# Kernel tuning notes

Hardware: AMD Instinct MI355X
Metric: run time of the kernel (lower is better)

## Reference

```python
import jax, jax.numpy as jnp
import numpy as np

NUM_HEADS = 2
ROPE_BASE = 10000.0


def _rope_tables(seq_len, head_dim, dtype):
    # inv_freq over even indices of head_dim
    inv_freq = 1.0 / (ROPE_BASE ** (jnp.arange(0, head_dim, 2, dtype=jnp.float32) / head_dim))
    t = jnp.arange(seq_len, dtype=jnp.float32)
    freqs = t[:, None] * inv_freq[None, :]            # (s, head_dim/2)
    emb = jnp.concatenate([freqs, freqs], axis=-1)    # (s, head_dim)
    return jnp.cos(emb).astype(dtype), jnp.sin(emb).astype(dtype)


def _apply_rotation(x_bsd, cos, sin):
    # x_bsd: (b, s, h*d); chunk in half along last dim (h=2 -> halves == head_dim)
    x1, x2 = jnp.split(x_bsd, 2, axis=-1)
    return jnp.concatenate([x1 * cos - x2 * sin, x2 * cos + x1 * sin], axis=-1)


def setup_inputs() -> dict:
    key = jax.random.key(0)
    k1, k2, k3, k4 = jax.random.split(key, 4)
    b, s, dim = 4, 2048, 2048
    x = jax.random.normal(k1, (b, s, dim), dtype=jnp.float32)
    wqkv = jax.random.normal(k2, (dim, 3 * dim), dtype=jnp.float32) * (dim ** -0.5)
    wout = jax.random.normal(k3, (dim, dim), dtype=jnp.float32) * (dim ** -0.5)
    bout = jax.random.normal(k4, (dim,), dtype=jnp.float32) * 0.01
    return {"x": x, "wqkv": wqkv, "wout": wout, "bout": bout}


def reference(x, wqkv, wout, bout):
    b, s, dim = x.shape
    h = NUM_HEADS
    d = dim // h
    scale = d ** -0.5

    qkv = x @ wqkv                                    # (b, s, 3*dim)
    qkv = qkv.reshape(b, s, 3, h, d).transpose(2, 0, 3, 1, 4)  # (3, b, h, s, d)
    q, k, v = qkv[0], qkv[1], qkv[2]                  # (b, h, s, d)

    # RoPE applied on (b, s, h*d) layout, exactly as source
    cos, sin = _rope_tables(s, d, x.dtype)            # (s, d) each
    q_flat = q.transpose(0, 2, 1, 3).reshape(b, s, h * d)
    k_flat = k.transpose(0, 2, 1, 3).reshape(b, s, h * d)
    q = _apply_rotation(q_flat, cos, sin).reshape(b, s, h, d).transpose(0, 2, 1, 3)
    k = _apply_rotation(k_flat, cos, sin).reshape(b, s, h, d).transpose(0, 2, 1, 3)

    scores = jnp.einsum('bhid,bhjd->bhij', q, k) * scale
    attn = jax.nn.softmax(scores, axis=-1)
    out = jnp.einsum('bhij,bhjd->bhid', attn, v)      # (b, h, s, d)
    out = out.transpose(0, 2, 1, 3).reshape(b, s, dim)
    return out @ wout + bout
```

## Files before the change

### kernel.cpp

```cpp
#include <hip/hip_runtime.h>
#include <hip/hip_fp16.h>

typedef __attribute__((ext_vector_type(4))) float f32x4;
typedef __attribute__((ext_vector_type(8))) _Float16 f16x8;
typedef __attribute__((ext_vector_type(4))) _Float16 f16x4;

__device__ __forceinline__ void gload_lds16(const void* gp, void* lp) {
    __builtin_amdgcn_global_load_lds(
        (const __attribute__((address_space(1))) void*)gp,
        (__attribute__((address_space(3))) void*)lp, 16, 0, 0);
}

__global__ void f32_to_f16_vec(const float* __restrict__ in, _Float16* __restrict__ out) {
    long i = ((long)blockIdx.x * 256 + threadIdx.x) * 4;
    f32x4 v = *(const f32x4*)(in + i);
    f16x4 h;
#pragma unroll
    for (int e = 0; e < 4; ++e) h[e] = (_Float16)v[e];
    *(f16x4*)(out + i) = h;
}

__global__ void transpose_f32_to_f16(const float* __restrict__ in, _Float16* __restrict__ out,
                                     int R, int C) {
    __shared__ _Float16 tile[32][36];
    const int c0 = blockIdx.x * 32, r0 = blockIdx.y * 32;
    const int t = threadIdx.x;
    const int r = t >> 3, c4 = (t & 7) * 4;
    f32x4 v = *(const f32x4*)(in + (long)(r0 + r) * C + c0 + c4);
    f16x4 h;
#pragma unroll
    for (int e = 0; e < 4; ++e) h[e] = (_Float16)v[e];
    *(f16x4*)&tile[r][c4] = h;
    __syncthreads();
    const int oc = t >> 3, o4 = (t & 7) * 4;
    f16x4 o;
#pragma unroll
    for (int e = 0; e < 4; ++e) o[e] = tile[o4 + e][oc];
    *(f16x4*)(out + (long)(c0 + oc) * R + r0 + o4) = o;
}

__global__ void rope_inplace(_Float16* __restrict__ qkv) {
    const int row = blockIdx.x;
    const int s = row & 2047;
    const int j0 = threadIdx.x * 4;
    _Float16* base = qkv + (long)row * 6144;
    f16x4 q0 = *(const f16x4*)(base + j0);
    f16x4 q1 = *(const f16x4*)(base + 1024 + j0);
    f16x4 k0 = *(const f16x4*)(base + 2048 + j0);
    f16x4 k1 = *(const f16x4*)(base + 3072 + j0);
    f16x4 oq0, oq1, ok0, ok1;
#pragma unroll
    for (int e = 0; e < 4; ++e) {
        int fi = (j0 + e) & 511;
        float expo = (float)(2 * fi) * (1.0f / 1024.0f);
        float invf = 1.0f / powf(10000.0f, expo);
        float ang = (float)s * invf;
        float sn, cs;
        sincosf(ang, &sn, &cs);
        float a = (float)q0[e], b = (float)q1[e];
        oq0[e] = (_Float16)(a * cs - b * sn);
        oq1[e] = (_Float16)(b * cs + a * sn);
        float c = (float)k0[e], d = (float)k1[e];
        ok0[e] = (_Float16)(c * cs - d * sn);
        ok1[e] = (_Float16)(d * cs + c * sn);
    }
    *(f16x4*)(base + j0) = oq0;
    *(f16x4*)(base + 1024 + j0) = oq1;
    *(f16x4*)(base + 2048 + j0) = ok0;
    *(f16x4*)(base + 3072 + j0) = ok1;
}

__global__ void v_transpose(const _Float16* __restrict__ qkv, _Float16* __restrict__ vT) {
    __shared__ _Float16 tile[32][36];
    const int z = blockIdx.z, b = z >> 1, h = z & 1;
    const int s0 = blockIdx.x * 32, d0 = blockIdx.y * 32;
    const int t = threadIdx.x;
    const int r = t >> 3, c4 = (t & 7) * 4;
    const _Float16* src = qkv + (long)(b * 2048 + s0 + r) * 6144 + 4096 + h * 1024 + d0 + c4;
    *(f16x4*)&tile[r][c4] = *(const f16x4*)src;
    __syncthreads();
    const int dr = t >> 3, sc = (t & 7) * 4;
    f16x4 o;
#pragma unroll
    for (int e = 0; e < 4; ++e) o[e] = tile[sc + e][dr];
    *(f16x4*)(vT + ((long)z * 1024 + d0 + dr) * 2048 + s0 + sc) = o;
}

__global__ __launch_bounds__(256) void softmax_rows_f32(float* __restrict__ S, float scale) {
    const int wid = threadIdx.x >> 6, lane = threadIdx.x & 63;
    const long row = (long)blockIdx.x * 4 + wid;
    float* rp = S + row * 2048;
    f32x4 v[8];
    float mx = -1e30f;
#pragma unroll
    for (int i = 0; i < 8; ++i) {
        v[i] = *(const f32x4*)(rp + (i * 64 + lane) * 4);
#pragma unroll
        for (int e = 0; e < 4; ++e) mx = fmaxf(mx, v[i][e]);
    }
#pragma unroll
    for (int o = 32; o > 0; o >>= 1) mx = fmaxf(mx, __shfl_xor(mx, o, 64));
    float sum = 0.f;
#pragma unroll
    for (int i = 0; i < 8; ++i)
#pragma unroll
        for (int e = 0; e < 4; ++e) {
            float p = __expf(scale * (v[i][e] - mx));
            v[i][e] = p; sum += p;
        }
#pragma unroll
    for (int o = 32; o > 0; o >>= 1) sum += __shfl_xor(sum, o, 64);
    float inv = 1.0f / sum;
    _Float16* wp = (_Float16*)S + row * 4096;
#pragma unroll
    for (int i = 0; i < 8; ++i) {
        f16x4 h;
#pragma unroll
        for (int e = 0; e < 4; ++e) h[e] = (_Float16)(v[i][e] * inv);
        *(f16x4*)(wp + (i * 64 + lane) * 4) = h;
    }
}

__global__ __launch_bounds__(256) void softmax_rows_f16(_Float16* __restrict__ S, float scale) {
    const int wid = threadIdx.x >> 6, lane = threadIdx.x & 63;
    const long row = (long)blockIdx.x * 4 + wid;
    _Float16* rp = S + row * 2048;
    f16x8 v[4];
    float f[32];
    float mx = -1e30f;
#pragma unroll
    for (int i = 0; i < 4; ++i) {
        v[i] = *(const f16x8*)(rp + i * 512 + lane * 8);
#pragma unroll
        for (int e = 0; e < 8; ++e) {
            f[i * 8 + e] = (float)v[i][e];
            mx = fmaxf(mx, f[i * 8 + e]);
        }
    }
#pragma unroll
    for (int o = 32; o > 0; o >>= 1) mx = fmaxf(mx, __shfl_xor(mx, o, 64));
    float sum = 0.f;
#pragma unroll
    for (int i = 0; i < 32; ++i) {
        float p = __expf(scale * (f[i] - mx));
        f[i] = p; sum += p;
    }
#pragma unroll
    for (int o = 32; o > 0; o >>= 1) sum += __shfl_xor(sum, o, 64);
    float inv = 1.0f / sum;
#pragma unroll
    for (int i = 0; i < 4; ++i) {
        f16x8 h;
#pragma unroll
        for (int e = 0; e < 8; ++e) h[e] = (_Float16)(f[i * 8 + e] * inv);
        *(f16x8*)(rp + i * 512 + lane * 8) = h;
    }
}

template <bool OUT_F16, bool BIAS>
__global__ __launch_bounds__(512, 2)
void gemm256(const _Float16* __restrict__ A, const _Float16* __restrict__ B,
             void* __restrict__ Cv, const float* __restrict__ bias,
             int K, int lda, int ldb, int ldc, int zmod,
             long a1, long a2, long b1, long b2, long c1, long c2) {
    __shared__ char lds[131072];
    const int z = blockIdx.z, zq = z / zmod, zr = z - zq * zmod;
    A += zq * a1 + zr * a2;
    B += zq * b1 + zr * b2;
    const long coff = zq * c1 + zr * c2;
    const int tm = blockIdx.y * 256, tn = blockIdx.x * 256;
    const int t = threadIdx.x;
    const int lane = t & 63, wid = t >> 6;
    const int wr = wid >> 2, wc = wid & 3;
    const int fr = lane & 15;

    const int scol = 8 * ((lane & 3) ^ ((lane >> 3) & 3));
    const int srow = wid * 32 + (lane >> 2);
    const _Float16* gA = A + (long)(tm + srow) * lda + scol;
    const _Float16* gB = B + (long)(tn + srow) * ldb + scol;
    char* lA = lds + wid * 2048;
    char* lB = lds + 65536 + wid * 2048;

    const int gsw = 16 * ((lane >> 4) ^ ((fr >> 1) & 3));
    const int aoff = (wr * 128 + fr) * 64 + gsw;
    const int boff = 65536 + (wc * 64 + fr) * 64 + gsw;

    const int NT = K >> 5;
    f32x4 acc[8][4] = {};

    auto stageA = [&](int tt) {
        const int so = (tt & 3) * 16384;
        const long ko = (long)tt * 32;
        gload_lds16(gA + ko, lA + so);
        gload_lds16(gA + ko + (long)16 * lda, lA + so + 1024);
    };
    auto stageB = [&](int tt) {
        const int so = (tt & 3) * 16384;
        const long ko = (long)tt * 32;
        gload_lds16(gB + ko, lB + so);
        gload_lds16(gB + ko + (long)16 * ldb, lB + so + 1024);
    };

    stageA(0); stageB(0); stageA(1); stageB(1); stageA(2); stageB(2);

    for (int tt = 0; tt < NT; ++tt) {
        if (tt + 3 <= NT)      asm volatile("s_waitcnt vmcnt(8)" ::: "memory");
        else if (tt + 2 == NT) asm volatile("s_waitcnt vmcnt(4)" ::: "memory");
        else                   asm volatile("s_waitcnt vmcnt(0)" ::: "memory");
        __builtin_amdgcn_s_barrier();
        __builtin_amdgcn_sched_barrier(0);
        const char* st = lds + (tt & 3) * 16384;
        f16x8 af[8], bf[4];
#pragma unroll
        for (int m = 0; m < 4; ++m) af[m] = *(const f16x8*)(st + aoff + m * 1024);
#pragma unroll
        for (int n = 0; n < 4; ++n) bf[n] = *(const f16x8*)(st + boff + n * 1024);
        if (tt + 3 < NT) stageA(tt + 3);
        __builtin_amdgcn_s_barrier();
        __builtin_amdgcn_sched_barrier(0);
        __builtin_amdgcn_s_setprio(1);
#pragma unroll
        for (int m = 0; m < 4; ++m)
#pragma unroll
            for (int n = 0; n < 4; ++n)
                acc[m][n] = __builtin_amdgcn_mfma_f32_16x16x32_f16(af[m], bf[n], acc[m][n], 0, 0, 0);
        __builtin_amdgcn_s_setprio(0);
#pragma unroll
        for (int m = 4; m < 8; ++m) af[m] = *(const f16x8*)(st + aoff + m * 1024);
        if (tt + 3 < NT) stageB(tt + 3);
        __builtin_amdgcn_s_barrier();
        __builtin_amdgcn_sched_barrier(0);
        __builtin_amdgcn_s_setprio(1);
#pragma unroll
        for (int m = 4; m < 8; ++m)
#pragma unroll
            for (int n = 0; n < 4; ++n)
                acc[m][n] = __builtin_amdgcn_mfma_f32_16x16x32_f16(af[m], bf[n], acc[m][n], 0, 0, 0);
        __builtin_amdgcn_s_setprio(0);
    }

    const int rb = tm + wr * 128 + (lane >> 4) * 4;
    const int cb = tn + wc * 64 + fr;
#pragma unroll
    for (int m = 0; m < 8; ++m) {
#pragma unroll
        for (int n = 0; n < 4; ++n) {
#pragma unroll
            for (int r = 0; r < 4; ++r) {
                float v = acc[m][n][r];
                const int row = rb + m * 16 + r;
                const int col = cb + n * 16;
                if (BIAS) v += bias[col];
                if (OUT_F16)
                    ((_Float16*)Cv)[coff + (long)row * ldc + col] = (_Float16)v;
                else
                    ((float*)Cv)[coff + (long)row * ldc + col] = v;
            }
        }
    }
}

extern "C" void kernel_launch(void* const* d_in, const int* in_sizes, int n_in,
                              void* d_out, int out_size, void* d_ws, size_t ws_size,
                              hipStream_t stream) {
    const float* x    = (const float*)d_in[0];
    const float* wqkv = (const float*)d_in[1];
    const float* wout = (const float*)d_in[2];
    const float* bout = (const float*)d_in[3];
    char* ws = (char*)d_ws;

    _Float16* qkv_h = (_Float16*)(ws);
    _Float16* x_h   = (_Float16*)(ws + 100663296);
    _Float16* wqkvT = (_Float16*)(ws + 134217728);
    _Float16* vT    = (_Float16*)(ws + 100663296);
    _Float16* woutT = (_Float16*)(ws);
    const bool batched = ws_size >= 234881024ULL;

    f32_to_f16_vec<<<dim3(16384), dim3(256), 0, stream>>>(x, x_h);
    transpose_f32_to_f16<<<dim3(192, 64), dim3(256), 0, stream>>>(wqkv, wqkvT, 2048, 6144);
    gemm256<true, false><<<dim3(24, 32, 1), dim3(512), 0, stream>>>(
        x_h, wqkvT, (void*)qkv_h, nullptr, 2048, 2048, 2048, 6144,
        1, 0L, 0L, 0L, 0L, 0L, 0L);
    rope_inplace<<<dim3(8192), dim3(256), 0, stream>>>(qkv_h);
    v_transpose<<<dim3(64, 32, 8), dim3(256), 0, stream>>>(qkv_h, vT);

    if (batched) {
        _Float16* S16  = (_Float16*)(ws + 134217728);
        _Float16* aout = (_Float16*)(ws + 201326592);
        gemm256<true, false><<<dim3(8, 8, 8), dim3(512), 0, stream>>>(
            qkv_h, qkv_h + 2048, (void*)S16, nullptr, 1024, 6144, 6144, 2048,
            2, 12582912L, 1024L, 12582912L, 1024L, 8388608L, 4194304L);
        softmax_rows_f16<<<dim3(4096), dim3(256), 0, stream>>>(S16, 0.03125f);
        gemm256<true, false><<<dim3(4, 8, 8), dim3(512), 0, stream>>>(
            S16, vT, (void*)aout, nullptr, 2048, 2048, 2048, 2048,
            2, 8388608L, 4194304L, 4194304L, 2097152L, 4194304L, 1024L);
        transpose_f32_to_f16<<<dim3(64, 64), dim3(256), 0, stream>>>(wout, woutT, 2048, 2048);
        gemm256<false, true><<<dim3(8, 32, 1), dim3(512), 0, stream>>>(
            aout, woutT, d_out, bout, 2048, 2048, 2048, 2048,
            1, 0L, 0L, 0L, 0L, 0L, 0L);
    } else {
        float*    S32  = (float*)(ws + 134217728);
        _Float16* aout = (_Float16*)(ws + 150994944);
        for (int z = 0; z < 8; ++z) {
            const _Float16* Az = qkv_h + (long)(z >> 1) * 12582912 + (z & 1) * 1024;
            gemm256<false, false><<<dim3(8, 8, 1), dim3(512), 0, stream>>>(
                Az, Az + 2048, (void*)S32, nullptr, 1024, 6144, 6144, 2048,
                1, 0L, 0L, 0L, 0L, 0L, 0L);
            softmax_rows_f32<<<dim3(512), dim3(256), 0, stream>>>(S32, 0.03125f);
            gemm256<true, false><<<dim3(4, 8, 1), dim3(512), 0, stream>>>(
                (const _Float16*)S32, vT + (long)z * 2097152,
                (void*)(aout + (long)(z >> 1) * 4194304 + (z & 1) * 1024), nullptr,
                2048, 4096, 2048, 2048, 1, 0L, 0L, 0L, 0L, 0L, 0L);
        }
        transpose_f32_to_f16<<<dim3(64, 64), dim3(256), 0, stream>>>(wout, woutT, 2048, 2048);
        gemm256<false, true><<<dim3(8, 32, 1), dim3(512), 0, stream>>>(
            aout, woutT, d_out, bout, 2048, 2048, 2048, 2048,
            1, 0L, 0L, 0L, 0L, 0L, 0L);
    }
}
```

Baseline: 548.9 us.

## Restructure gemm256 mainloop to K=64 double-buffered tiles with quadrant-split MFMA phases

The 256x256 GEMM mainloop moves from a 4-stage ring of K=32 tiles to a 2-stage double buffer of K=64 tiles, with a new XOR swizzle matched to 128-byte rows. Each iteration is split into four quadrant MFMA phases that reuse A and B fragments across phases. The half-tile async loads for the next A and the tile after next of B are interleaved between those phases. The aim is fewer barriers and waits per unit of K and better overlap of global-to-LDS copies with MFMA work. The cost is more barriers per iteration and a tighter vmcnt accounting that could leave the pipeline shallower or mis-synchronised.

```diff
diff --git a/kernel.cpp b/kernel.cpp
--- a/kernel.cpp
+++ b/kernel.cpp
@@ -172,71 +172,120 @@
     const int t = threadIdx.x;
     const int lane = t & 63, wid = t >> 6;
     const int wr = wid >> 2, wc = wid & 3;
-    const int fr = lane & 15;
-
-    const int scol = 8 * ((lane & 3) ^ ((lane >> 3) & 3));
-    const int srow = wid * 32 + (lane >> 2);
-    const _Float16* gA = A + (long)(tm + srow) * lda + scol;
-    const _Float16* gB = B + (long)(tn + srow) * ldb + scol;
-    char* lA = lds + wid * 2048;
-    char* lB = lds + 65536 + wid * 2048;
-
-    const int gsw = 16 * ((lane >> 4) ^ ((fr >> 1) & 3));
-    const int aoff = (wr * 128 + fr) * 64 + gsw;
-    const int boff = 65536 + (wc * 64 + fr) * 64 + gsw;
-
-    const int NT = K >> 5;
+    const int fr = lane & 15, kg = lane >> 4;
+
+    const int strow = wid * 16 + (lane >> 3);
+    const int stcol = ((lane & 7) ^ (lane >> 3)) * 8;
+    const _Float16* gA = A + (long)(tm + strow) * lda + stcol;
+    const _Float16* gB = B + (long)(tn + strow) * ldb + stcol;
+    char* const ldsw = lds + wid * 2048;
+
+    const int sw0 = 16 * ((0 * 4 + kg) ^ (fr & 7));
+    const int sw1 = 16 * ((1 * 4 + kg) ^ (fr & 7));
+
+    const int NT = K >> 6;
     f32x4 acc[8][4] = {};
 
-    auto stageA = [&](int tt) {
-        const int so = (tt & 3) * 16384;
-        const long ko = (long)tt * 32;
-        gload_lds16(gA + ko, lA + so);
-        gload_lds16(gA + ko + (long)16 * lda, lA + so + 1024);
+    auto stageA = [&](int tt, int h) {
+        const _Float16* s = gA + (long)(h * 128) * lda + tt * 64;
+        char* d = ldsw + (tt & 1) * 65536 + h * 16384;
+        gload_lds16(s, d);
+        gload_lds16(s + (long)8 * lda, d + 1024);
     };
-    auto stageB = [&](int tt) {
-        const int so = (tt & 3) * 16384;
-        const long ko = (long)tt * 32;
-        gload_lds16(gB + ko, lB + so);
-        gload_lds16(gB + ko + (long)16 * ldb, lB + so + 1024);
+    auto stageB = [&](int tt, int h) {
+        const _Float16* s = gB + (long)(h * 128) * ldb + tt * 64;
+        char* d = ldsw + (tt & 1) * 65536 + 32768 + h * 16384;
+        gload_lds16(s, d);
+        gload_lds16(s + (long)8 * ldb, d + 1024);
     };
 
-    stageA(0); stageB(0); stageA(1); stageB(1); stageA(2); stageB(2);
-
-    for (int tt = 0; tt < NT; ++tt) {
-        if (tt + 3 <= NT)      asm volatile("s_waitcnt vmcnt(8)" ::: "memory");
-        else if (tt + 2 == NT) asm volatile("s_waitcnt vmcnt(4)" ::: "memory");
-        else                   asm volatile("s_waitcnt vmcnt(0)" ::: "memory");
-        __builtin_amdgcn_s_barrier();
-        __builtin_amdgcn_sched_barrier(0);
-        const char* st = lds + (tt & 3) * 16384;
-        f16x8 af[8], bf[4];
-#pragma unroll
-        for (int m = 0; m < 4; ++m) af[m] = *(const f16x8*)(st + aoff + m * 1024);
-#pragma unroll
-        for (int n = 0; n < 4; ++n) bf[n] = *(const f16x8*)(st + boff + n * 1024);
-        if (tt + 3 < NT) stageA(tt + 3);
-        __builtin_amdgcn_s_barrier();
+    stageB(0, 0); stageB(0, 1); stageA(0, 0); stageA(0, 1);
+    stageB(1, 0); stageB(1, 1);
+    asm volatile("s_waitcnt vmcnt(4)" ::: "memory");
+    __builtin_amdgcn_s_barrier();
+
+    f16x8 af[4][2], bf0[2][2], bf1[2][2];
+    const int arow = (wr * 128 + fr) * 128;
+    const int brow = 32768 + (wc * 64 + fr) * 128;
+
+    for (int g = 0; g < NT; ++g) {
+        const char* buf = lds + (g & 1) * 65536;
+#pragma unroll
+        for (int m = 0; m < 4; ++m) {
+            af[m][0] = *(const f16x8*)(buf + arow + m * 2048 + sw0);
+            af[m][1] = *(const f16x8*)(buf + arow + m * 2048 + sw1);
+        }
+#pragma unroll
+        for (int n = 0; n < 2; ++n) {
+            bf0[n][0] = *(const f16x8*)(buf + brow + n * 2048 + sw0);
+            bf0[n][1] = *(const f16x8*)(buf + brow + n * 2048 + sw1);
+        }
+        if (g + 1 < NT) stageA(g + 1, 0);
+        __builtin_amdgcn_s_barrier();
+        asm volatile("s_waitcnt lgkmcnt(0)" ::: "memory");
         __builtin_amdgcn_sched_barrier(0);
         __builtin_amdgcn_s_setprio(1);
 #pragma unroll
         for (int m = 0; m < 4; ++m)
 #pragma unroll
-            for (int n = 0; n < 4; ++n)
-                acc[m][n] = __builtin_amdgcn_mfma_f32_16x16x32_f16(af[m], bf[n], acc[m][n], 0, 0, 0);
+            for (int n = 0; n < 2; ++n)
+#pragma unroll
+                for (int k = 0; k < 2; ++k)
+                    acc[m][n] = __builtin_amdgcn_mfma_f32_16x16x32_f16(af[m][k], bf0[n][k], acc[m][n], 0, 0, 0);
         __builtin_amdgcn_s_setprio(0);
-#pragma unroll
-        for (int m = 4; m < 8; ++m) af[m] = *(const f16x8*)(st + aoff + m * 1024);
-        if (tt + 3 < NT) stageB(tt + 3);
-        __builtin_amdgcn_s_barrier();
+        __builtin_amdgcn_s_barrier();
+#pragma unroll
+        for (int n = 0; n < 2; ++n) {
+            bf1[n][0] = *(const f16x8*)(buf + brow + 4096 + n * 2048 + sw0);
+            bf1[n][1] = *(const f16x8*)(buf + brow + 4096 + n * 2048 + sw1);
+        }
+        if (g + 1 < NT) stageA(g + 1, 1);
+        __builtin_amdgcn_s_barrier();
+        asm volatile("s_waitcnt lgkmcnt(0)" ::: "memory");
         __builtin_amdgcn_sched_barrier(0);
         __builtin_amdgcn_s_setprio(1);
 #pragma unroll
-        for (int m = 4; m < 8; ++m)
-#pragma unroll
-            for (int n = 0; n < 4; ++n)
-                acc[m][n] = __builtin_amdgcn_mfma_f32_16x16x32_f16(af[m], bf[n], acc[m][n], 0, 0, 0);
+        for (int m = 0; m < 4; ++m)
+#pragma unroll
+            for (int n = 0; n < 2; ++n)
+#pragma unroll
+                for (int k = 0; k < 2; ++k)
+                    acc[m][n + 2] = __builtin_amdgcn_mfma_f32_16x16x32_f16(af[m][k], bf1[n][k], acc[m][n + 2], 0, 0, 0);
         __builtin_amdgcn_s_setprio(0);
+        __builtin_amdgcn_s_barrier();
+#pragma unroll
+        for (int m = 0; m < 4; ++m) {
+            af[m][0] = *(const f16x8*)(buf + arow + 8192 + m * 2048 + sw0);
+            af[m][1] = *(const f16x8*)(buf + arow + 8192 + m * 2048 + sw1);
+        }
+        if (g + 2 < NT) stageB(g + 2, 0);
+        __builtin_amdgcn_s_barrier();
+        asm volatile("s_waitcnt lgkmcnt(0)" ::: "memory");
+        __builtin_amdgcn_sched_barrier(0);
+        __builtin_amdgcn_s_setprio(1);
+#pragma unroll
+        for (int m = 0; m < 4; ++m)
+#pragma unroll
+            for (int n = 0; n < 2; ++n)
+#pragma unroll
+                for (int k = 0; k < 2; ++k)
+                    acc[m + 4][n + 2] = __builtin_amdgcn_mfma_f32_16x16x32_f16(af[m][k], bf1[n][k], acc[m + 4][n + 2], 0, 0, 0);
+        __builtin_amdgcn_s_setprio(0);
+        __builtin_amdgcn_s_barrier();
+        if (g + 2 < NT) stageB(g + 2, 1);
+        __builtin_amdgcn_s_barrier();
+        __builtin_amdgcn_s_setprio(1);
+#pragma unroll
+        for (int m = 0; m < 4; ++m)
+#pragma unroll
+            for (int n = 0; n < 2; ++n)
+#pragma unroll
+                for (int k = 0; k < 2; ++k)
+                    acc[m + 4][n] = __builtin_amdgcn_mfma_f32_16x16x32_f16(af[m][k], bf0[n][k], acc[m + 4][n], 0, 0, 0);
+        __builtin_amdgcn_s_setprio(0);
+        if (g + 2 < NT)      asm volatile("s_waitcnt vmcnt(4)" ::: "memory");
+        else if (g + 1 < NT) asm volatile("s_waitcnt vmcnt(0)" ::: "memory");
+        __builtin_amdgcn_s_barrier();
     }
 
     const int rb = tm + wr * 128 + (lane >> 4) * 4;
```

New measurement: 536.1 us. -2.3%, faster.

## Retile GEMM to 256x128 with 4 waves, triple-buffer LDS; precompute RoPE tables

Applied to the files above, without the earlier changes.

Replaces the 512-thread 256x256 GEMM with a 256-thread 256x128 tile. It uses a 3-slot LDS ring buffer with prefetch distance 2 and one barrier per k-step instead of split A/B staging with three barriers. Grids are doubled along N to match. RoPE now reads precomputed cos/sin tables built by a separate kernel instead of calling powf/sincosf per element. The trade-off is less B reuse per tile and more blocks, in exchange for smaller LDS use, higher occupancy and fewer syncs.

```diff
diff --git a/kernel.cpp b/kernel.cpp
--- a/kernel.cpp
+++ b/kernel.cpp
@@ -9,6 +9,17 @@
     __builtin_amdgcn_global_load_lds(
         (const __attribute__((address_space(1))) void*)gp,
         (__attribute__((address_space(3))) void*)lp, 16, 0, 0);
+}
+
+__global__ void rope_tables_k(float* __restrict__ cosT, float* __restrict__ sinT) {
+    int idx = blockIdx.x * 256 + threadIdx.x;
+    int s = idx >> 9, j = idx & 511;
+    float invf = exp2f(-13.287712379549449f * (float)j * (1.0f / 512.0f));
+    float ang = (float)s * invf;
+    float sn, cs;
+    sincosf(ang, &sn, &cs);
+    cosT[idx] = cs;
+    sinT[idx] = sn;
 }
 
 __global__ void f32_to_f16_vec(const float* __restrict__ in, _Float16* __restrict__ out) {
@@ -39,7 +50,8 @@
     *(f16x4*)(out + (long)(c0 + oc) * R + r0 + o4) = o;
 }
 
-__global__ void rope_inplace(_Float16* __restrict__ qkv) {
+__global__ void rope_inplace(_Float16* __restrict__ qkv, const float* __restrict__ cosT,
+                             const float* __restrict__ sinT) {
     const int row = blockIdx.x;
     const int s = row & 2047;
     const int j0 = threadIdx.x * 4;
@@ -48,21 +60,18 @@
     f16x4 q1 = *(const f16x4*)(base + 1024 + j0);
     f16x4 k0 = *(const f16x4*)(base + 2048 + j0);
     f16x4 k1 = *(const f16x4*)(base + 3072 + j0);
+    const int jj = j0 & 511;
+    f32x4 cs = *(const f32x4*)(cosT + (long)s * 512 + jj);
+    f32x4 sn = *(const f32x4*)(sinT + (long)s * 512 + jj);
     f16x4 oq0, oq1, ok0, ok1;
 #pragma unroll
     for (int e = 0; e < 4; ++e) {
-        int fi = (j0 + e) & 511;
-        float expo = (float)(2 * fi) * (1.0f / 1024.0f);
-        float invf = 1.0f / powf(10000.0f, expo);
-        float ang = (float)s * invf;
-        float sn, cs;
-        sincosf(ang, &sn, &cs);
         float a = (float)q0[e], b = (float)q1[e];
-        oq0[e] = (_Float16)(a * cs - b * sn);
-        oq1[e] = (_Float16)(b * cs + a * sn);
+        oq0[e] = (_Float16)(a * cs[e] - b * sn[e]);
+        oq1[e] = (_Float16)(b * cs[e] + a * sn[e]);
         float c = (float)k0[e], d = (float)k1[e];
-        ok0[e] = (_Float16)(c * cs - d * sn);
-        ok1[e] = (_Float16)(d * cs + c * sn);
+        ok0[e] = (_Float16)(c * cs[e] - d * sn[e]);
+        ok1[e] = (_Float16)(d * cs[e] + c * sn[e]);
     }
     *(f16x4*)(base + j0) = oq0;
     *(f16x4*)(base + 1024 + j0) = oq1;
@@ -158,85 +167,70 @@
 }
 
 template <bool OUT_F16, bool BIAS>
-__global__ __launch_bounds__(512, 2)
-void gemm256(const _Float16* __restrict__ A, const _Float16* __restrict__ B,
+__global__ __launch_bounds__(256, 2)
+void gemm_rg(const _Float16* __restrict__ A, const _Float16* __restrict__ B,
              void* __restrict__ Cv, const float* __restrict__ bias,
              int K, int lda, int ldb, int ldc, int zmod,
              long a1, long a2, long b1, long b2, long c1, long c2) {
-    __shared__ char lds[131072];
+    __shared__ char lds[73728];
     const int z = blockIdx.z, zq = z / zmod, zr = z - zq * zmod;
     A += zq * a1 + zr * a2;
     B += zq * b1 + zr * b2;
     const long coff = zq * c1 + zr * c2;
-    const int tm = blockIdx.y * 256, tn = blockIdx.x * 256;
+    const int tm = blockIdx.y * 256, tn = blockIdx.x * 128;
     const int t = threadIdx.x;
     const int lane = t & 63, wid = t >> 6;
-    const int wr = wid >> 2, wc = wid & 3;
-    const int fr = lane & 15;
-
-    const int scol = 8 * ((lane & 3) ^ ((lane >> 3) & 3));
-    const int srow = wid * 32 + (lane >> 2);
-    const _Float16* gA = A + (long)(tm + srow) * lda + scol;
-    const _Float16* gB = B + (long)(tn + srow) * ldb + scol;
-    char* lA = lds + wid * 2048;
-    char* lB = lds + 65536 + wid * 2048;
-
-    const int gsw = 16 * ((lane >> 4) ^ ((fr >> 1) & 3));
-    const int aoff = (wr * 128 + fr) * 64 + gsw;
-    const int boff = 65536 + (wc * 64 + fr) * 64 + gsw;
+    const int wr = wid >> 1, wc = wid & 1;
+    const int fr = lane & 15, kg = lane >> 4;
+
+    const int strow = t >> 2;
+    const int stcol = 8 * ((t & 3) ^ ((t >> 3) & 3));
+    const _Float16* gA = A + (long)(tm + strow) * lda + stcol;
+    const _Float16* gB = B + (long)(tn + strow) * ldb + stcol;
+    const int ldsw = wid * 1024;
+
+    const int swz = 16 * (kg ^ ((fr >> 1) & 3));
+    const int arow = (wr * 128 + fr) * 64 + swz;
+    const int brow = 16384 + (wc * 64 + fr) * 64 + swz;
 
     const int NT = K >> 5;
     f32x4 acc[8][4] = {};
 
-    auto stageA = [&](int tt) {
-        const int so = (tt & 3) * 16384;
+    auto stage = [&](int tt, int slot) {
         const long ko = (long)tt * 32;
-        gload_lds16(gA + ko, lA + so);
-        gload_lds16(gA + ko + (long)16 * lda, lA + so + 1024);
+        char* d = lds + slot * 24576 + ldsw;
+#pragma unroll
+        for (int i = 0; i < 4; ++i)
+            gload_lds16(gA + ko + (long)(i * 64) * lda, d + i * 4096);
+#pragma unroll
+        for (int i = 0; i < 2; ++i)
+            gload_lds16(gB + ko + (long)(i * 64) * ldb, d + 16384 + i * 4096);
     };
-    auto stageB = [&](int tt) {
-        const int so = (tt & 3) * 16384;
-        const long ko = (long)tt * 32;
-        gload_lds16(gB + ko, lB + so);
-        gload_lds16(gB + ko + (long)16 * ldb, lB + so + 1024);
-    };
-
-    stageA(0); stageB(0); stageA(1); stageB(1); stageA(2); stageB(2);
-
+
+    stage(0, 0);
+    stage(1, 1);
+
+    int st = 0, sp = 2;
     for (int tt = 0; tt < NT; ++tt) {
-        if (tt + 3 <= NT)      asm volatile("s_waitcnt vmcnt(8)" ::: "memory");
-        else if (tt + 2 == NT) asm volatile("s_waitcnt vmcnt(4)" ::: "memory");
-        else                   asm volatile("s_waitcnt vmcnt(0)" ::: "memory");
+        if (tt + 1 < NT) asm volatile("s_waitcnt vmcnt(6)" ::: "memory");
+        else             asm volatile("s_waitcnt vmcnt(0)" ::: "memory");
         __builtin_amdgcn_s_barrier();
-        __builtin_amdgcn_sched_barrier(0);
-        const char* st = lds + (tt & 3) * 16384;
+        const char* buf = lds + st * 24576;
         f16x8 af[8], bf[4];
 #pragma unroll
-        for (int m = 0; m < 4; ++m) af[m] = *(const f16x8*)(st + aoff + m * 1024);
-#pragma unroll
-        for (int n = 0; n < 4; ++n) bf[n] = *(const f16x8*)(st + boff + n * 1024);
-        if (tt + 3 < NT) stageA(tt + 3);
-        __builtin_amdgcn_s_barrier();
-        __builtin_amdgcn_sched_barrier(0);
+        for (int m = 0; m < 8; ++m) af[m] = *(const f16x8*)(buf + arow + m * 1024);
+#pragma unroll
+        for (int n = 0; n < 4; ++n) bf[n] = *(const f16x8*)(buf + brow + n * 1024);
+        if (tt + 2 < NT) stage(tt + 2, sp);
         __builtin_amdgcn_s_setprio(1);
 #pragma unroll
-        for (int m = 0; m < 4; ++m)
+        for (int m = 0; m < 8; ++m)
 #pragma unroll
             for (int n = 0; n < 4; ++n)
                 acc[m][n] = __builtin_amdgcn_mfma_f32_16x16x32_f16(af[m], bf[n], acc[m][n], 0, 0, 0);
         __builtin_amdgcn_s_setprio(0);
-#pragma unroll
-        for (int m = 4; m < 8; ++m) af[m] = *(const f16x8*)(st + aoff + m * 1024);
-        if (tt + 3 < NT) stageB(tt + 3);
-        __builtin_amdgcn_s_barrier();
-        __builtin_amdgcn_sched_barrier(0);
-        __builtin_amdgcn_s_setprio(1);
-#pragma unroll
-        for (int m = 4; m < 8; ++m)
-#pragma unroll
-            for (int n = 0; n < 4; ++n)
-                acc[m][n] = __builtin_amdgcn_mfma_f32_16x16x32_f16(af[m], bf[n], acc[m][n], 0, 0, 0);
-        __builtin_amdgcn_s_setprio(0);
+        st = (st == 2) ? 0 : st + 1;
+        sp = (sp == 2) ? 0 : sp + 1;
     }
 
     const int rb = tm + wr * 128 + (lane >> 4) * 4;
@@ -273,29 +267,32 @@
     _Float16* x_h   = (_Float16*)(ws + 100663296);
     _Float16* wqkvT = (_Float16*)(ws + 134217728);
     _Float16* vT    = (_Float16*)(ws + 100663296);
+    float*    cosT  = (float*)(ws + 100663296);
+    float*    sinT  = (float*)(ws + 104857600);
     _Float16* woutT = (_Float16*)(ws);
     const bool batched = ws_size >= 234881024ULL;
 
     f32_to_f16_vec<<<dim3(16384), dim3(256), 0, stream>>>(x, x_h);
     transpose_f32_to_f16<<<dim3(192, 64), dim3(256), 0, stream>>>(wqkv, wqkvT, 2048, 6144);
-    gemm256<true, false><<<dim3(24, 32, 1), dim3(512), 0, stream>>>(
+    gemm_rg<true, false><<<dim3(48, 32, 1), dim3(256), 0, stream>>>(
         x_h, wqkvT, (void*)qkv_h, nullptr, 2048, 2048, 2048, 6144,
         1, 0L, 0L, 0L, 0L, 0L, 0L);
-    rope_inplace<<<dim3(8192), dim3(256), 0, stream>>>(qkv_h);
+    rope_tables_k<<<dim3(4096), dim3(256), 0, stream>>>(cosT, sinT);
+    rope_inplace<<<dim3(8192), dim3(256), 0, stream>>>(qkv_h, cosT, sinT);
     v_transpose<<<dim3(64, 32, 8), dim3(256), 0, stream>>>(qkv_h, vT);
 
     if (batched) {
         _Float16* S16  = (_Float16*)(ws + 134217728);
         _Float16* aout = (_Float16*)(ws + 201326592);
-        gemm256<true, false><<<dim3(8, 8, 8), dim3(512), 0, stream>>>(
+        gemm_rg<true, false><<<dim3(16, 8, 8), dim3(256), 0, stream>>>(
             qkv_h, qkv_h + 2048, (void*)S16, nullptr, 1024, 6144, 6144, 2048,
             2, 12582912L, 1024L, 12582912L, 1024L, 8388608L, 4194304L);
         softmax_rows_f16<<<dim3(4096), dim3(256), 0, stream>>>(S16, 0.03125f);
-        gemm256<true, false><<<dim3(4, 8, 8), dim3(512), 0, stream>>>(
+        gemm_rg<true, false><<<dim3(8, 8, 8), dim3(256), 0, stream>>>(
             S16, vT, (void*)aout, nullptr, 2048, 2048, 2048, 2048,
             2, 8388608L, 4194304L, 4194304L, 2097152L, 4194304L, 1024L);
         transpose_f32_to_f16<<<dim3(64, 64), dim3(256), 0, stream>>>(wout, woutT, 2048, 2048);
-        gemm256<false, true><<<dim3(8, 32, 1), dim3(512), 0, stream>>>(
+        gemm_rg<false, true><<<dim3(16, 32, 1), dim3(256), 0, stream>>>(
             aout, woutT, d_out, bout, 2048, 2048, 2048, 2048,
             1, 0L, 0L, 0L, 0L, 0L, 0L);
     } else {
@@ -303,17 +300,17 @@
         _Float16* aout = (_Float16*)(ws + 150994944);
         for (int z = 0; z < 8; ++z) {
             const _Float16* Az = qkv_h + (long)(z >> 1) * 12582912 + (z & 1) * 1024;
-            gemm256<false, false><<<dim3(8, 8, 1), dim3(512), 0, stream>>>(
+            gemm_rg<false, false><<<dim3(16, 8, 1), dim3(256), 0, stream>>>(
                 Az, Az + 2048, (void*)S32, nullptr, 1024, 6144, 6144, 2048,
                 1, 0L, 0L, 0L, 0L, 0L, 0L);
             softmax_rows_f32<<<dim3(512), dim3(256), 0, stream>>>(S32, 0.03125f);
-            gemm256<true, false><<<dim3(4, 8, 1), dim3(512), 0, stream>>>(
+            gemm_rg<true, false><<<dim3(8, 8, 1), dim3(256), 0, stream>>>(
                 (const _Float16*)S32, vT + (long)z * 2097152,
                 (void*)(aout + (long)(z >> 1) * 4194304 + (z & 1) * 1024), nullptr,
                 2048, 4096, 2048, 2048, 1, 0L, 0L, 0L, 0L, 0L, 0L);
         }
         transpose_f32_to_f16<<<dim3(64, 64), dim3(256), 0, stream>>>(wout, woutT, 2048, 2048);
-        gemm256<false, true><<<dim3(8, 32, 1), dim3(512), 0, stream>>>(
+        gemm_rg<false, true><<<dim3(16, 32, 1), dim3(256), 0, stream>>>(
             aout, woutT, d_out, bout, 2048, 2048, 2048, 2048,
             1, 0L, 0L, 0L, 0L, 0L, 0L);
     }
```

New measurement: 565.8 us. 1.03x slower.
